# Optimization experiments

Measured on AMD Instinct MI355X. Metric: run time of the kernel, lower is better.

The kernel has to match this reference:

```python
import jax, jax.numpy as jnp
import numpy as np

# dims: batch B, seq T, model C, expert hidden H, num experts E, top-k K
B, T, C, H, E, K = 4, 1024, 1024, 1024, 8, 2


def _swiglu(x):
    a, b = jnp.split(x, 2, axis=-1)
    return jax.nn.silu(a) * b


def setup_inputs() -> dict:
    key = jax.random.key(0)
    ks = jax.random.split(key, 6)
    s = 0.02
    x = jax.random.normal(ks[0], (B, T, C), jnp.float32)
    # weights stored [in, out] (transpose of torch Linear layout; same math y = x @ W)
    w_shared_in = jax.random.normal(ks[1], (C, 2 * H), jnp.float32) * s
    w_shared_out = jax.random.normal(ks[2], (H, C), jnp.float32) * s
    w1_shared = jax.random.normal(ks[3], (C, 2 * H), jnp.float32) * s
    w2 = jax.random.normal(ks[4], (E, H, C), jnp.float32) * s  # stacked routed_w2
    w_gate = jax.random.normal(ks[5], (C, E), jnp.float32) * s
    gate_bias = jnp.zeros((E,), jnp.float32)  # buffer, updated only in training
    return {
        "x": x,
        "w_shared_in": w_shared_in,
        "w_shared_out": w_shared_out,
        "w1_shared": w1_shared,
        "w2": w2,
        "w_gate": w_gate,
        "gate_bias": gate_bias,
    }


def reference(x, w_shared_in, w_shared_out, w1_shared, w2, w_gate, gate_bias):
    Bx, Tx, Cx = x.shape
    S = Bx * Tx
    fx = x.reshape(S, Cx)  # [S, C]

    # shared expert: SwiGLU MLP
    shared_out = _swiglu(fx @ w_shared_in) @ w_shared_out  # [S, C]

    # router: softmax(top-k) over biased logits
    logits = fx @ w_gate + gate_bias  # [S, E]
    probs = jax.nn.softmax(logits, axis=-1)
    top_val, top_idx = jax.lax.top_k(probs, K)  # [S, K]

    # dense dispatch-weight matrix [S, E] (zero where expert not selected)
    wdense = jnp.zeros((S, E), probs.dtype).at[
        jnp.arange(S)[:, None], top_idx
    ].add(top_val)

    # routed experts share w1_shared, so the SwiGLU hidden is identical for all
    # experts; compute it once for every token, then apply per-expert w2.
    hid = _swiglu(fx @ w1_shared)  # [S, H]
    routed_out = jnp.zeros_like(shared_out)
    for e in range(E):  # small fixed expert count
        routed_out = routed_out + wdense[:, e:e + 1] * (hid @ w2[e])

    return (shared_out + routed_out).reshape(Bx, Tx, Cx)
```

## Files before the change

kernel.cpp:

```cpp
#include <hip/hip_runtime.h>
#include <stdint.h>

typedef __attribute__((ext_vector_type(4))) float f32x4;
typedef __attribute__((ext_vector_type(8))) short s16x8;

static constexpr int S_TOK = 4096;
static constexpr int CDIM  = 1024;
static constexpr int HDIM  = 1024;
static constexpr int H2    = 2048;
static constexpr int NEXP  = 8;

#define MAXRT2 40

__device__ __forceinline__ unsigned short f2bf(float f) {
  union { float f; uint32_t u; } c; c.f = f;
  uint32_t u = c.u;
  u += 0x7fffu + ((u >> 16) & 1u);
  return (unsigned short)(u >> 16);
}

__device__ __forceinline__ float bf2f(unsigned short u) {
  return __uint_as_float(((uint32_t)u) << 16);
}

__device__ __forceinline__ void gload16(const void* g, void* l) {
  __builtin_amdgcn_global_load_lds(
      (const __attribute__((address_space(1))) void*)g,
      (__attribute__((address_space(3))) void*)l, 16, 0, 0);
}

__global__ __launch_bounds__(256) void prep_kernel(
    const float* __restrict__ wsi, const float* __restrict__ w1s,
    const float* __restrict__ wso, const float* __restrict__ w2,
    unsigned short* __restrict__ w12i, unsigned short* __restrict__ wso_t,
    unsigned short* __restrict__ w2t) {
  __shared__ float t[32][33];
  const int b = blockIdx.x;
  const int tid = threadIdx.x;

  if (b < 4096) {
    const float* src = (b >= 2048) ? w1s : wsi;
    const int halfoff = (b >= 2048) ? 2048 : 0;
    const int rem = b & 2047;
    const int r0 = (rem >> 6) * 32;
    const int c0 = (rem & 63) * 32;
#pragma unroll
    for (int i = 0; i < 4; ++i) {
      int idx = tid + i * 256;
      int r = idx >> 5, c = idx & 31;
      t[r][c] = src[(size_t)(r0 + r) * H2 + c0 + c];
    }
    __syncthreads();
#pragma unroll
    for (int i = 0; i < 4; ++i) {
      int idx = tid + i * 256;
      int r = idx >> 5, c = idx & 31;
      const int ccol = c0 + r;
      const int part = ccol >> 10, h = ccol & 1023;
      const int drow = halfoff + (h & 15) + ((h >> 4) << 5) + (part << 4);
      w12i[(size_t)drow * CDIM + r0 + c] = f2bf(t[c][r]);
    }
    return;
  }
  const float* src;
  unsigned short* dst;
  int bx, by;
  if (b < 5120) {
    const int b3 = b - 4096;
    src = wso; dst = wso_t; by = b3 >> 5; bx = b3 & 31;
  } else {
    const int b4 = b - 5120;
    const int z = b4 >> 10;
    const int rem = b4 & 1023;
    src = w2 + (size_t)z * HDIM * CDIM;
    dst = w2t + (size_t)z * HDIM * CDIM;
    by = rem >> 5; bx = rem & 31;
  }
  const int r0 = by * 32, c0 = bx * 32;
#pragma unroll
  for (int i = 0; i < 4; ++i) {
    int idx = tid + i * 256;
    int r = idx >> 5, c = idx & 31;
    t[r][c] = src[(size_t)(r0 + r) * CDIM + c0 + c];
  }
  __syncthreads();
#pragma unroll
  for (int i = 0; i < 4; ++i) {
    int idx = tid + i * 256;
    int r = idx >> 5, c = idx & 31;
    dst[(size_t)(c0 + r) * HDIM + r0 + c] = f2bf(t[c][r]);
  }
}

__global__ void router_kernel(const float* __restrict__ x, const float* __restrict__ wg,
                              const float* __restrict__ gb,
                              int2* __restrict__ ti_e, float2* __restrict__ ti_w,
                              unsigned short* __restrict__ xb) {
  const int l = threadIdx.x & 63;
  const int wid = threadIdx.x >> 6;
  const int s = blockIdx.x * 4 + wid;
  const float* xr = x + (size_t)s * CDIM;
  unsigned short* xbr = xb + (size_t)s * CDIM;
  float acc[NEXP];
#pragma unroll
  for (int e = 0; e < NEXP; ++e) acc[e] = 0.f;
#pragma unroll
  for (int c4 = 0; c4 < CDIM / 4; c4 += 64) {
    const int i4 = c4 + l;
    const float4 xv = reinterpret_cast<const float4*>(xr)[i4];
    ushort4 o;
    o.x = f2bf(xv.x); o.y = f2bf(xv.y); o.z = f2bf(xv.z); o.w = f2bf(xv.w);
    reinterpret_cast<ushort4*>(xbr)[i4] = o;
    const float* wr_ = wg + (size_t)i4 * 4 * NEXP;
#pragma unroll
    for (int e = 0; e < NEXP; ++e)
      acc[e] += xv.x * wr_[e] + xv.y * wr_[e + NEXP] +
                xv.z * wr_[e + 2 * NEXP] + xv.w * wr_[e + 3 * NEXP];
  }
#pragma unroll
  for (int e = 0; e < NEXP; ++e) {
#pragma unroll
    for (int off = 32; off > 0; off >>= 1) acc[e] += __shfl_xor(acc[e], off);
    acc[e] += gb[e];
  }
  float m = acc[0];
#pragma unroll
  for (int e = 1; e < NEXP; ++e) m = fmaxf(m, acc[e]);
  float ex[NEXP], sum = 0.f;
#pragma unroll
  for (int e = 0; e < NEXP; ++e) { ex[e] = __expf(acc[e] - m); sum += ex[e]; }
  int i0 = 0;
#pragma unroll
  for (int e = 1; e < NEXP; ++e) if (acc[e] > acc[i0]) i0 = e;
  int i1 = (i0 == 0) ? 1 : 0;
#pragma unroll
  for (int e = 0; e < NEXP; ++e) {
    if (e == i0) continue;
    if (acc[e] > acc[i1]) i1 = e;
  }
  if (l == 0) {
    const float inv = 1.f / sum;
    ti_e[s] = make_int2(i0, i1);
    ti_w[s] = make_float2(ex[i0] * inv, ex[i1] * inv);
  }
}

__global__ __launch_bounds__(1024) void build_kernel(
    const int2* __restrict__ ti_e,
    int* __restrict__ cnt, int* __restrict__ offs,
    int* __restrict__ gidx, int2* __restrict__ ti_slot) {
  __shared__ int gcnt[64][NEXP];
  __shared__ int gbase[64][NEXP];
  __shared__ int eoff[NEXP];
  const int tid = threadIdx.x;
  const int wid = tid >> 6, lane = tid & 63;

  for (int p = 0; p < 4; ++p) {
    const int g = p * 16 + wid;
    const int2 e = ti_e[g * 64 + lane];
#pragma unroll
    for (int ex = 0; ex < NEXP; ++ex) {
      uint64_t b0 = __ballot(e.x == ex);
      uint64_t b1 = __ballot(e.y == ex);
      if (lane == 0) gcnt[g][ex] = __popcll(b0) + __popcll(b1);
    }
  }
  __syncthreads();
  if (tid < NEXP) {
    const int ex = tid;
    int a = 0;
    for (int g = 0; g < 64; ++g) { gbase[g][ex] = a; a += gcnt[g][ex]; }
    eoff[ex] = a;
  }
  __syncthreads();
  if (tid == 0) {
    int a = 0;
#pragma unroll
    for (int ex = 0; ex < NEXP; ++ex) {
      const int c = eoff[ex];
      offs[ex] = a; cnt[ex] = c; eoff[ex] = a; a += c;
    }
    offs[NEXP] = a;
  }
  __syncthreads();
  for (int p = 0; p < 4; ++p) {
    const int g = p * 16 + wid;
    const int s = g * 64 + lane;
    const int2 e = ti_e[s];
    const uint64_t below = (lane == 0) ? 0ull : (~0ull >> (64 - lane));
    const uint64_t beloweq = below | (1ull << lane);
    int slot0 = 0, slot1 = 0;
#pragma unroll
    for (int ex = 0; ex < NEXP; ++ex) {
      uint64_t b0 = __ballot(e.x == ex);
      uint64_t b1 = __ballot(e.y == ex);
      const int base = gbase[g][ex];
      if (e.x == ex) slot0 = base + __popcll(b0 & below) + __popcll(b1 & below);
      if (e.y == ex) slot1 = base + __popcll(b0 & beloweq) + __popcll(b1 & below);
    }
    ti_slot[s] = make_int2(slot0, slot1);
    gidx[eoff[e.x] + slot0] = s;
    gidx[eoff[e.y] + slot1] = s;
  }
}

__global__ __launch_bounds__(256, 4) void gemm1_kernel(
    const unsigned short* __restrict__ xb, const unsigned short* __restrict__ w12i,
    unsigned short* __restrict__ Hs, unsigned short* __restrict__ Hr) {
  __shared__ unsigned short As[128 * 32];
  __shared__ unsigned short Bs[128 * 32];
  const int tid = threadIdx.x;
  const int l = tid & 63, wid = tid >> 6;
  const int wr = wid >> 1, wc = wid & 1;
  const int lr = l & 15, lk = (l >> 4) << 3;
  const int hw = blockIdx.y * gridDim.x + blockIdx.x;
  const int logical = (hw & 7) * 128 + (hw >> 3);
  const int m0 = (logical >> 5) * 128;
  const int n0 = (logical & 31) * 128;
  f32x4 acc[4][4] = {};
  const unsigned short* ga0 = xb + (size_t)(m0 + (tid >> 2)) * CDIM + ((tid & 3) << 3);
  const unsigned short* ga1 = ga0 + (size_t)64 * CDIM;
  const unsigned short* gb0 = w12i + (size_t)(n0 + (tid >> 2)) * CDIM + ((tid & 3) << 3);
  const unsigned short* gb1 = gb0 + (size_t)64 * CDIM;

  for (int k0 = 0; k0 < 1024; k0 += 32) {
    gload16(ga0 + k0, As + tid * 8);
    gload16(ga1 + k0, As + 2048 + tid * 8);
    gload16(gb0 + k0, Bs + tid * 8);
    gload16(gb1 + k0, Bs + 2048 + tid * 8);
    __syncthreads();
    s16x8 a[4], b[4];
#pragma unroll
    for (int fm = 0; fm < 4; ++fm)
      a[fm] = *reinterpret_cast<const s16x8*>(As + (wr * 64 + fm * 16 + lr) * 32 + lk);
#pragma unroll
    for (int fn = 0; fn < 4; ++fn)
      b[fn] = *reinterpret_cast<const s16x8*>(Bs + (wc * 64 + fn * 16 + lr) * 32 + lk);
#pragma unroll
    for (int fm = 0; fm < 4; ++fm)
#pragma unroll
      for (int fn = 0; fn < 4; ++fn)
        acc[fm][fn] = __builtin_amdgcn_mfma_f32_16x16x32_bf16(a[fm], b[fn], acc[fm][fn], 0, 0, 0);
    __syncthreads();
  }

  unsigned short* Hbuf = (n0 < 2048) ? Hs : Hr;
  const int rb = m0 + wr * 64 + ((l >> 4) << 2);
  const int hb0 = ((n0 & 2047) >> 1) + wc * 32;
#pragma unroll
  for (int fm = 0; fm < 4; ++fm)
#pragma unroll
    for (int j = 0; j < 2; ++j)
#pragma unroll
      for (int r = 0; r < 4; ++r) {
        float a = acc[fm][2 * j][r];
        float b = acc[fm][2 * j + 1][r];
        float hv = (a / (1.f + __expf(-a))) * b;
        Hbuf[(size_t)(rb + fm * 16 + r) * HDIM + hb0 + j * 16 + lr] = f2bf(hv);
      }
}

__global__ __launch_bounds__(512) void gemm2_kernel(
    const unsigned short* __restrict__ Hs, const unsigned short* __restrict__ Hr,
    const unsigned short* __restrict__ wso_t, const unsigned short* __restrict__ w2t,
    const int* __restrict__ cnt, const int* __restrict__ offs, const int* __restrict__ gidx,
    unsigned short* __restrict__ Dout, unsigned short* __restrict__ Eout) {
  __shared__ unsigned short SA[4][2][4096];
  __shared__ unsigned short SB[4][2][4096];
  const int tid = threadIdx.x;
  const int l = tid & 63, wid = tid >> 6;
  const int wm = wid >> 2, wn = wid & 3;
  const int lr = l & 15;
  const int hi8 = (l >> 4) << 3;
  const int wnh = wn >> 1;
  const int wno = (wn & 1) << 6;
  const int hw = blockIdx.y * gridDim.x + blockIdx.x;
  const int logical = (hw & 7) * 28 + (hw >> 3);
  const int gx = logical >> 2;
  const int n0 = (logical & 3) * 256;
  f32x4 acc[8][4] = {};

  const int srow = tid >> 2;
  const int cs = (((tid & 3) ^ ((tid >> 3) & 3)) << 3);

  const unsigned short *pa0, *pa1, *pb0, *pb1;
  int e = 0, cnte = 0, mt = 0, base = 0;
  const bool dense = (gx < 16);
  if (dense) {
    const int m0 = gx * 256;
    pa0 = Hs + (size_t)(m0 + srow) * HDIM + cs;
    pa1 = pa0 + (size_t)128 * HDIM;
    pb0 = wso_t + (size_t)(n0 + srow) * HDIM + cs;
    pb1 = pb0 + (size_t)128 * HDIM;
  } else {
    int t = gx - 16;
    bool found = false;
#pragma unroll
    for (int ee = 0; ee < NEXP; ++ee) {
      int c = cnt[ee];
      int nt = (c + 255) >> 8;
      if (!found) {
        if (t < nt) { e = ee; cnte = c; found = true; }
        else t -= nt;
      }
    }
    if (!found) return;
    mt = t;
    base = offs[e];
    const int r0 = mt * 256 + srow;
    const int tok0 = gidx[base + min(r0, cnte - 1)];
    const int tok1 = gidx[base + min(r0 + 128, cnte - 1)];
    pa0 = Hr + (size_t)tok0 * HDIM + cs;
    pa1 = Hr + (size_t)tok1 * HDIM + cs;
    pb0 = w2t + (size_t)e * CDIM * HDIM + (size_t)(n0 + srow) * HDIM + cs;
    pb1 = pb0 + (size_t)128 * HDIM;
  }

  const int t8 = tid * 8;
#pragma unroll
  for (int s = 0; s < 3; ++s) {
    const int kk = s * 32;
    gload16(pa0 + kk, &SA[s][0][t8]);
    gload16(pa1 + kk, &SA[s][1][t8]);
    gload16(pb0 + kk, &SB[s][0][t8]);
    gload16(pb1 + kk, &SB[s][1][t8]);
  }

  for (int s = 0; s < 32; ++s) {
    if (s < 30)       asm volatile("s_waitcnt vmcnt(8)" ::: "memory");
    else if (s == 30) asm volatile("s_waitcnt vmcnt(4)" ::: "memory");
    else              asm volatile("s_waitcnt vmcnt(0)" ::: "memory");
    __builtin_amdgcn_s_barrier();
    asm volatile("" ::: "memory");
    const int c = s & 3;
    const unsigned short* A_ = &SA[c][wm][0];
    const unsigned short* B_ = &SB[c][wnh][0];
    s16x8 a[8], b[4];
#pragma unroll
    for (int f = 0; f < 8; ++f) {
      const int r = f * 16 + lr;
      a[f] = *reinterpret_cast<const s16x8*>(&A_[r * 32 + (hi8 ^ (((r >> 1) & 3) << 3))]);
    }
#pragma unroll
    for (int j = 0; j < 4; ++j) {
      const int r = wno + j * 16 + lr;
      b[j] = *reinterpret_cast<const s16x8*>(&B_[r * 32 + (hi8 ^ (((r >> 1) & 3) << 3))]);
    }
    const int c3 = (s + 3) & 3;
    const int kk = (s + 3) * 32;
    const bool st = (s <= 28);
    if (st) gload16(pa0 + kk, &SA[c3][0][t8]);
    __builtin_amdgcn_s_setprio(1);
#pragma unroll
    for (int f = 0; f < 4; ++f) {
      acc[f][0] = __builtin_amdgcn_mfma_f32_16x16x32_bf16(a[f], b[0], acc[f][0], 0, 0, 0);
      acc[f][1] = __builtin_amdgcn_mfma_f32_16x16x32_bf16(a[f], b[1], acc[f][1], 0, 0, 0);
    }
    __builtin_amdgcn_s_setprio(0);
    if (st) gload16(pa1 + kk, &SA[c3][1][t8]);
    __builtin_amdgcn_s_setprio(1);
#pragma unroll
    for (int f = 0; f < 4; ++f) {
      acc[f][2] = __builtin_amdgcn_mfma_f32_16x16x32_bf16(a[f], b[2], acc[f][2], 0, 0, 0);
      acc[f][3] = __builtin_amdgcn_mfma_f32_16x16x32_bf16(a[f], b[3], acc[f][3], 0, 0, 0);
    }
    __builtin_amdgcn_s_setprio(0);
    if (st) gload16(pb0 + kk, &SB[c3][0][t8]);
    __builtin_amdgcn_s_setprio(1);
#pragma unroll
    for (int f = 0; f < 4; ++f) {
      acc[4 + f][0] = __builtin_amdgcn_mfma_f32_16x16x32_bf16(a[4 + f], b[0], acc[4 + f][0], 0, 0, 0);
      acc[4 + f][1] = __builtin_amdgcn_mfma_f32_16x16x32_bf16(a[4 + f], b[1], acc[4 + f][1], 0, 0, 0);
    }
    __builtin_amdgcn_s_setprio(0);
    if (st) gload16(pb1 + kk, &SB[c3][1][t8]);
    __builtin_amdgcn_s_setprio(1);
#pragma unroll
    for (int f = 0; f < 4; ++f) {
      acc[4 + f][2] = __builtin_amdgcn_mfma_f32_16x16x32_bf16(a[4 + f], b[2], acc[4 + f][2], 0, 0, 0);
      acc[4 + f][3] = __builtin_amdgcn_mfma_f32_16x16x32_bf16(a[4 + f], b[3], acc[4 + f][3], 0, 0, 0);
    }
    __builtin_amdgcn_s_setprio(0);
  }

  const int rloc0 = wm * 128 + ((l >> 4) << 2);
  const int cb = n0 + wn * 64 + lr;
  if (dense) {
    const int rb = gx * 256 + rloc0;
#pragma unroll
    for (int fm = 0; fm < 8; ++fm)
#pragma unroll
      for (int fn = 0; fn < 4; ++fn)
#pragma unroll
        for (int r = 0; r < 4; ++r)
          Dout[(size_t)(rb + fm * 16 + r) * CDIM + cb + fn * 16] = f2bf(acc[fm][fn][r]);
  } else {
#pragma unroll
    for (int fm = 0; fm < 8; ++fm)
#pragma unroll
      for (int fn = 0; fn < 4; ++fn)
#pragma unroll
        for (int r = 0; r < 4; ++r) {
          const int rloc = mt * 256 + rloc0 + fm * 16 + r;
          if (rloc < cnte)
            Eout[(size_t)(base + rloc) * CDIM + cb + fn * 16] = f2bf(acc[fm][fn][r]);
        }
  }
}

__global__ void scatter_kernel(float* __restrict__ out, const unsigned short* __restrict__ Dout,
                               const unsigned short* __restrict__ Eout,
                               const int2* __restrict__ ti_e, const int2* __restrict__ ti_slot,
                               const float2* __restrict__ ti_w, const int* __restrict__ offs) {
  const int total = S_TOK * (CDIM / 8);
  int i = blockIdx.x * blockDim.x + threadIdx.x;
  const int st = gridDim.x * blockDim.x;
  for (; i < total; i += st) {
    const int s = i >> 7;
    const int j = (i & 127) << 3;
    const int2 e = ti_e[s];
    const int2 sl = ti_slot[s];
    const float2 wv = ti_w[s];
    const int p0 = offs[e.x] + sl.x;
    const int p1 = offs[e.y] + sl.y;
    const ushort4* d0 = reinterpret_cast<const ushort4*>(Dout + (size_t)s * CDIM + j);
    const ushort4* e0 = reinterpret_cast<const ushort4*>(Eout + (size_t)p0 * CDIM + j);
    const ushort4* e1 = reinterpret_cast<const ushort4*>(Eout + (size_t)p1 * CDIM + j);
    float* op = out + (size_t)s * CDIM + j;
#pragma unroll
    for (int q = 0; q < 2; ++q) {
      ushort4 dd = d0[q], a = e0[q], b = e1[q];
      float4 o;
      o.x = bf2f(dd.x) + wv.x * bf2f(a.x) + wv.y * bf2f(b.x);
      o.y = bf2f(dd.y) + wv.x * bf2f(a.y) + wv.y * bf2f(b.y);
      o.z = bf2f(dd.z) + wv.x * bf2f(a.z) + wv.y * bf2f(b.z);
      o.w = bf2f(dd.w) + wv.x * bf2f(a.w) + wv.y * bf2f(b.w);
      reinterpret_cast<float4*>(op)[q] = o;
    }
  }
}

extern "C" void kernel_launch(void* const* d_in, const int* in_sizes, int n_in,
                              void* d_out, int out_size, void* d_ws, size_t ws_size,
                              hipStream_t stream) {
  (void)in_sizes; (void)n_in; (void)out_size; (void)ws_size;
  const float* x   = (const float*)d_in[0];
  const float* wsi = (const float*)d_in[1];
  const float* wso = (const float*)d_in[2];
  const float* w1s = (const float*)d_in[3];
  const float* w2  = (const float*)d_in[4];
  const float* wg  = (const float*)d_in[5];
  const float* gb  = (const float*)d_in[6];
  float* out = (float*)d_out;

  char* w = (char*)d_ws;
  auto alloc = [&](size_t bytes) {
    char* p = w; w += (bytes + 255) & ~(size_t)255; return p;
  };
  unsigned short* xb    = (unsigned short*)alloc((size_t)S_TOK * CDIM * 2);
  unsigned short* w12i  = (unsigned short*)alloc((size_t)2 * H2 * CDIM * 2);
  unsigned short* wso_t = (unsigned short*)alloc((size_t)CDIM * HDIM * 2);
  unsigned short* w2t   = (unsigned short*)alloc((size_t)NEXP * CDIM * HDIM * 2);
  unsigned short* Hs    = (unsigned short*)alloc((size_t)S_TOK * HDIM * 2);
  unsigned short* Hr    = (unsigned short*)alloc((size_t)S_TOK * HDIM * 2);
  unsigned short* Dout  = (unsigned short*)alloc((size_t)S_TOK * CDIM * 2);
  unsigned short* Eout  = (unsigned short*)alloc((size_t)2 * S_TOK * CDIM * 2);
  int2*   ti_e   = (int2*)alloc((size_t)S_TOK * 8);
  int2*   ti_slot= (int2*)alloc((size_t)S_TOK * 8);
  float2* ti_w   = (float2*)alloc((size_t)S_TOK * 8);
  int*    cnt    = (int*)alloc(64);
  int*    offs   = (int*)alloc(64);
  int*    gidx   = (int*)alloc((size_t)2 * S_TOK * 4);

  router_kernel<<<S_TOK / 4, 256, 0, stream>>>(x, wg, gb, ti_e, ti_w, xb);
  build_kernel<<<1, 1024, 0, stream>>>(ti_e, cnt, offs, gidx, ti_slot);

  prep_kernel<<<13312, 256, 0, stream>>>(wsi, w1s, wso, w2, w12i, wso_t, w2t);

  gemm1_kernel<<<dim3(32, 32), 256, 0, stream>>>(xb, w12i, Hs, Hr);

  gemm2_kernel<<<dim3(16 + MAXRT2, CDIM / 256), 512, 0, stream>>>(
      Hs, Hr, wso_t, w2t, cnt, offs, gidx, Dout, Eout);

  scatter_kernel<<<2048, 256, 0, stream>>>(out, Dout, Eout, ti_e, ti_slot, ti_w, offs);
}
```

Baseline: 128.3 us.

## Move gemm1 onto the pipelined 256x256 gemm2 core and simplify router loads

Factors the 4-stage, swizzled-LDS, prefetch-interleaved MFMA main loop out of gemm2 into a shared device function. gemm1 now uses it with 256x256 tiles, 512 threads and a 16x16 grid, replacing its 128x128 single-buffered loop that waited on barriers every k-step. The aim is more overlap of global loads with MFMA work and more reuse per tile, at the cost of far fewer blocks (256) and possibly lower occupancy. The router loop also switches from float4 loads to scalar per-element loads, which may reduce load efficiency.

```diff
diff --git a/kernel.cpp b/kernel.cpp
--- a/kernel.cpp
+++ b/kernel.cpp
@@ -104,18 +104,12 @@
   float acc[NEXP];
 #pragma unroll
   for (int e = 0; e < NEXP; ++e) acc[e] = 0.f;
-#pragma unroll
-  for (int c4 = 0; c4 < CDIM / 4; c4 += 64) {
-    const int i4 = c4 + l;
-    const float4 xv = reinterpret_cast<const float4*>(xr)[i4];
-    ushort4 o;
-    o.x = f2bf(xv.x); o.y = f2bf(xv.y); o.z = f2bf(xv.z); o.w = f2bf(xv.w);
-    reinterpret_cast<ushort4*>(xbr)[i4] = o;
-    const float* wr_ = wg + (size_t)i4 * 4 * NEXP;
-#pragma unroll
-    for (int e = 0; e < NEXP; ++e)
-      acc[e] += xv.x * wr_[e] + xv.y * wr_[e + NEXP] +
-                xv.z * wr_[e + 2 * NEXP] + xv.w * wr_[e + 3 * NEXP];
+  for (int c = l; c < CDIM; c += 64) {
+    float xv = xr[c];
+    xbr[c] = f2bf(xv);
+    const float* wr_ = wg + (size_t)c * NEXP;
+#pragma unroll
+    for (int e = 0; e < NEXP; ++e) acc[e] += xv * wr_[e];
   }
 #pragma unroll
   for (int e = 0; e < NEXP; ++e) {
@@ -204,59 +198,118 @@
   }
 }
 
-__global__ __launch_bounds__(256, 4) void gemm1_kernel(
+__device__ __forceinline__ void core_d3(
+    const unsigned short* pa0, const unsigned short* pa1,
+    const unsigned short* pb0, const unsigned short* pb1,
+    unsigned short* SA, unsigned short* SB,
+    int tid, int wm, int wnh, int wno, int lr, int hi8,
+    f32x4 (&acc)[8][4]) {
+  const int t8 = tid * 8;
+#pragma unroll
+  for (int s = 0; s < 3; ++s) {
+    const int kk = s * 32;
+    gload16(pa0 + kk, SA + s * 8192 + t8);
+    gload16(pa1 + kk, SA + s * 8192 + 4096 + t8);
+    gload16(pb0 + kk, SB + s * 8192 + t8);
+    gload16(pb1 + kk, SB + s * 8192 + 4096 + t8);
+  }
+  for (int s = 0; s < 32; ++s) {
+    if (s < 30)       asm volatile("s_waitcnt vmcnt(8)" ::: "memory");
+    else if (s == 30) asm volatile("s_waitcnt vmcnt(4)" ::: "memory");
+    else              asm volatile("s_waitcnt vmcnt(0)" ::: "memory");
+    __builtin_amdgcn_s_barrier();
+    asm volatile("" ::: "memory");
+    const int c = s & 3;
+    const unsigned short* A_ = SA + c * 8192 + wm * 4096;
+    const unsigned short* B_ = SB + c * 8192 + wnh * 4096;
+    s16x8 a[8], b[4];
+#pragma unroll
+    for (int f = 0; f < 8; ++f) {
+      const int r = f * 16 + lr;
+      a[f] = *reinterpret_cast<const s16x8*>(&A_[r * 32 + (hi8 ^ (((r >> 1) & 3) << 3))]);
+    }
+#pragma unroll
+    for (int j = 0; j < 4; ++j) {
+      const int r = wno + j * 16 + lr;
+      b[j] = *reinterpret_cast<const s16x8*>(&B_[r * 32 + (hi8 ^ (((r >> 1) & 3) << 3))]);
+    }
+    const int c3 = (s + 3) & 3;
+    const int kk = (s + 3) * 32;
+    const bool st = (s <= 28);
+    if (st) gload16(pa0 + kk, SA + c3 * 8192 + t8);
+    __builtin_amdgcn_s_setprio(1);
+#pragma unroll
+    for (int f = 0; f < 4; ++f) {
+      acc[f][0] = __builtin_amdgcn_mfma_f32_16x16x32_bf16(a[f], b[0], acc[f][0], 0, 0, 0);
+      acc[f][1] = __builtin_amdgcn_mfma_f32_16x16x32_bf16(a[f], b[1], acc[f][1], 0, 0, 0);
+    }
+    __builtin_amdgcn_s_setprio(0);
+    if (st) gload16(pa1 + kk, SA + c3 * 8192 + 4096 + t8);
+    __builtin_amdgcn_s_setprio(1);
+#pragma unroll
+    for (int f = 0; f < 4; ++f) {
+      acc[f][2] = __builtin_amdgcn_mfma_f32_16x16x32_bf16(a[f], b[2], acc[f][2], 0, 0, 0);
+      acc[f][3] = __builtin_amdgcn_mfma_f32_16x16x32_bf16(a[f], b[3], acc[f][3], 0, 0, 0);
+    }
+    __builtin_amdgcn_s_setprio(0);
+    if (st) gload16(pb0 + kk, SB + c3 * 8192 + t8);
+    __builtin_amdgcn_s_setprio(1);
+#pragma unroll
+    for (int f = 0; f < 4; ++f) {
+      acc[4 + f][0] = __builtin_amdgcn_mfma_f32_16x16x32_bf16(a[4 + f], b[0], acc[4 + f][0], 0, 0, 0);
+      acc[4 + f][1] = __builtin_amdgcn_mfma_f32_16x16x32_bf16(a[4 + f], b[1], acc[4 + f][1], 0, 0, 0);
+    }
+    __builtin_amdgcn_s_setprio(0);
+    if (st) gload16(pb1 + kk, SB + c3 * 8192 + 4096 + t8);
+    __builtin_amdgcn_s_setprio(1);
+#pragma unroll
+    for (int f = 0; f < 4; ++f) {
+      acc[4 + f][2] = __builtin_amdgcn_mfma_f32_16x16x32_bf16(a[4 + f], b[2], acc[4 + f][2], 0, 0, 0);
+      acc[4 + f][3] = __builtin_amdgcn_mfma_f32_16x16x32_bf16(a[4 + f], b[3], acc[4 + f][3], 0, 0, 0);
+    }
+    __builtin_amdgcn_s_setprio(0);
+  }
+}
+
+__global__ __launch_bounds__(512) void gemm1_kernel(
     const unsigned short* __restrict__ xb, const unsigned short* __restrict__ w12i,
     unsigned short* __restrict__ Hs, unsigned short* __restrict__ Hr) {
-  __shared__ unsigned short As[128 * 32];
-  __shared__ unsigned short Bs[128 * 32];
+  __shared__ unsigned short SA[4 * 2 * 4096];
+  __shared__ unsigned short SB[4 * 2 * 4096];
   const int tid = threadIdx.x;
   const int l = tid & 63, wid = tid >> 6;
-  const int wr = wid >> 1, wc = wid & 1;
-  const int lr = l & 15, lk = (l >> 4) << 3;
+  const int wm = wid >> 2, wn = wid & 3;
+  const int lr = l & 15;
+  const int hi8 = (l >> 4) << 3;
+  const int wnh = wn >> 1;
+  const int wno = (wn & 1) << 6;
   const int hw = blockIdx.y * gridDim.x + blockIdx.x;
-  const int logical = (hw & 7) * 128 + (hw >> 3);
-  const int m0 = (logical >> 5) * 128;
-  const int n0 = (logical & 31) * 128;
-  f32x4 acc[4][4] = {};
-  const unsigned short* ga0 = xb + (size_t)(m0 + (tid >> 2)) * CDIM + ((tid & 3) << 3);
-  const unsigned short* ga1 = ga0 + (size_t)64 * CDIM;
-  const unsigned short* gb0 = w12i + (size_t)(n0 + (tid >> 2)) * CDIM + ((tid & 3) << 3);
-  const unsigned short* gb1 = gb0 + (size_t)64 * CDIM;
-
-  for (int k0 = 0; k0 < 1024; k0 += 32) {
-    gload16(ga0 + k0, As + tid * 8);
-    gload16(ga1 + k0, As + 2048 + tid * 8);
-    gload16(gb0 + k0, Bs + tid * 8);
-    gload16(gb1 + k0, Bs + 2048 + tid * 8);
-    __syncthreads();
-    s16x8 a[4], b[4];
-#pragma unroll
-    for (int fm = 0; fm < 4; ++fm)
-      a[fm] = *reinterpret_cast<const s16x8*>(As + (wr * 64 + fm * 16 + lr) * 32 + lk);
-#pragma unroll
-    for (int fn = 0; fn < 4; ++fn)
-      b[fn] = *reinterpret_cast<const s16x8*>(Bs + (wc * 64 + fn * 16 + lr) * 32 + lk);
-#pragma unroll
-    for (int fm = 0; fm < 4; ++fm)
-#pragma unroll
-      for (int fn = 0; fn < 4; ++fn)
-        acc[fm][fn] = __builtin_amdgcn_mfma_f32_16x16x32_bf16(a[fm], b[fn], acc[fm][fn], 0, 0, 0);
-    __syncthreads();
-  }
+  const int logical = (hw & 7) * 32 + (hw >> 3);
+  const int m0 = (logical >> 4) * 256;
+  const int n0 = (logical & 15) * 256;
+  const int srow = tid >> 2;
+  const int cs = (((tid & 3) ^ ((tid >> 3) & 3)) << 3);
+  f32x4 acc[8][4] = {};
+  const unsigned short* pa0 = xb + (size_t)(m0 + srow) * CDIM + cs;
+  const unsigned short* pa1 = pa0 + (size_t)128 * CDIM;
+  const unsigned short* pb0 = w12i + (size_t)(n0 + srow) * CDIM + cs;
+  const unsigned short* pb1 = pb0 + (size_t)128 * CDIM;
+
+  core_d3(pa0, pa1, pb0, pb1, SA, SB, tid, wm, wnh, wno, lr, hi8, acc);
 
   unsigned short* Hbuf = (n0 < 2048) ? Hs : Hr;
-  const int rb = m0 + wr * 64 + ((l >> 4) << 2);
-  const int hb0 = ((n0 & 2047) >> 1) + wc * 32;
-#pragma unroll
-  for (int fm = 0; fm < 4; ++fm)
+  const int rb = m0 + wm * 128 + ((l >> 4) << 2);
+  const int hbase = ((n0 & 2047) >> 1) + wn * 32;
+#pragma unroll
+  for (int fm = 0; fm < 8; ++fm)
 #pragma unroll
     for (int j = 0; j < 2; ++j)
 #pragma unroll
       for (int r = 0; r < 4; ++r) {
-        float a = acc[fm][2 * j][r];
-        float b = acc[fm][2 * j + 1][r];
-        float hv = (a / (1.f + __expf(-a))) * b;
-        Hbuf[(size_t)(rb + fm * 16 + r) * HDIM + hb0 + j * 16 + lr] = f2bf(hv);
+        float av = acc[fm][2 * j][r];
+        float bv = acc[fm][2 * j + 1][r];
+        float hv = (av / (1.f + __expf(-av))) * bv;
+        Hbuf[(size_t)(rb + fm * 16 + r) * HDIM + hbase + j * 16 + lr] = f2bf(hv);
       }
 }
 
@@ -265,8 +318,8 @@
     const unsigned short* __restrict__ wso_t, const unsigned short* __restrict__ w2t,
     const int* __restrict__ cnt, const int* __restrict__ offs, const int* __restrict__ gidx,
     unsigned short* __restrict__ Dout, unsigned short* __restrict__ Eout) {
-  __shared__ unsigned short SA[4][2][4096];
-  __shared__ unsigned short SB[4][2][4096];
+  __shared__ unsigned short SA[4 * 2 * 4096];
+  __shared__ unsigned short SB[4 * 2 * 4096];
   const int tid = threadIdx.x;
   const int l = tid & 63, wid = tid >> 6;
   const int wm = wid >> 2, wn = wid & 3;
@@ -316,72 +369,7 @@
     pb1 = pb0 + (size_t)128 * HDIM;
   }
 
-  const int t8 = tid * 8;
-#pragma unroll
-  for (int s = 0; s < 3; ++s) {
-    const int kk = s * 32;
-    gload16(pa0 + kk, &SA[s][0][t8]);
-    gload16(pa1 + kk, &SA[s][1][t8]);
-    gload16(pb0 + kk, &SB[s][0][t8]);
-    gload16(pb1 + kk, &SB[s][1][t8]);
-  }
-
-  for (int s = 0; s < 32; ++s) {
-    if (s < 30)       asm volatile("s_waitcnt vmcnt(8)" ::: "memory");
-    else if (s == 30) asm volatile("s_waitcnt vmcnt(4)" ::: "memory");
-    else              asm volatile("s_waitcnt vmcnt(0)" ::: "memory");
-    __builtin_amdgcn_s_barrier();
-    asm volatile("" ::: "memory");
-    const int c = s & 3;
-    const unsigned short* A_ = &SA[c][wm][0];
-    const unsigned short* B_ = &SB[c][wnh][0];
-    s16x8 a[8], b[4];
-#pragma unroll
-    for (int f = 0; f < 8; ++f) {
-      const int r = f * 16 + lr;
-      a[f] = *reinterpret_cast<const s16x8*>(&A_[r * 32 + (hi8 ^ (((r >> 1) & 3) << 3))]);
-    }
-#pragma unroll
-    for (int j = 0; j < 4; ++j) {
-      const int r = wno + j * 16 + lr;
-      b[j] = *reinterpret_cast<const s16x8*>(&B_[r * 32 + (hi8 ^ (((r >> 1) & 3) << 3))]);
-    }
-    const int c3 = (s + 3) & 3;
-    const int kk = (s + 3) * 32;
-    const bool st = (s <= 28);
-    if (st) gload16(pa0 + kk, &SA[c3][0][t8]);
-    __builtin_amdgcn_s_setprio(1);
-#pragma unroll
-    for (int f = 0; f < 4; ++f) {
-      acc[f][0] = __builtin_amdgcn_mfma_f32_16x16x32_bf16(a[f], b[0], acc[f][0], 0, 0, 0);
-      acc[f][1] = __builtin_amdgcn_mfma_f32_16x16x32_bf16(a[f], b[1], acc[f][1], 0, 0, 0);
-    }
-    __builtin_amdgcn_s_setprio(0);
-    if (st) gload16(pa1 + kk, &SA[c3][1][t8]);
-    __builtin_amdgcn_s_setprio(1);
-#pragma unroll
-    for (int f = 0; f < 4; ++f) {
-      acc[f][2] = __builtin_amdgcn_mfma_f32_16x16x32_bf16(a[f], b[2], acc[f][2], 0, 0, 0);
-      acc[f][3] = __builtin_amdgcn_mfma_f32_16x16x32_bf16(a[f], b[3], acc[f][3], 0, 0, 0);
-    }
-    __builtin_amdgcn_s_setprio(0);
-    if (st) gload16(pb0 + kk, &SB[c3][0][t8]);
-    __builtin_amdgcn_s_setprio(1);
-#pragma unroll
-    for (int f = 0; f < 4; ++f) {
-      acc[4 + f][0] = __builtin_amdgcn_mfma_f32_16x16x32_bf16(a[4 + f], b[0], acc[4 + f][0], 0, 0, 0);
-      acc[4 + f][1] = __builtin_amdgcn_mfma_f32_16x16x32_bf16(a[4 + f], b[1], acc[4 + f][1], 0, 0, 0);
-    }
-    __builtin_amdgcn_s_setprio(0);
-    if (st) gload16(pb1 + kk, &SB[c3][1][t8]);
-    __builtin_amdgcn_s_setprio(1);
-#pragma unroll
-    for (int f = 0; f < 4; ++f) {
-      acc[4 + f][2] = __builtin_amdgcn_mfma_f32_16x16x32_bf16(a[4 + f], b[2], acc[4 + f][2], 0, 0, 0);
-      acc[4 + f][3] = __builtin_amdgcn_mfma_f32_16x16x32_bf16(a[4 + f], b[3], acc[4 + f][3], 0, 0, 0);
-    }
-    __builtin_amdgcn_s_setprio(0);
-  }
+  core_d3(pa0, pa1, pb0, pb1, SA, SB, tid, wm, wnh, wno, lr, hi8, acc);
 
   const int rloc0 = wm * 128 + ((l >> 4) << 2);
   const int cb = n0 + wn * 64 + lr;
@@ -477,7 +465,7 @@
 
   prep_kernel<<<13312, 256, 0, stream>>>(wsi, w1s, wso, w2, w12i, wso_t, w2t);
 
-  gemm1_kernel<<<dim3(32, 32), 256, 0, stream>>>(xb, w12i, Hs, Hr);
+  gemm1_kernel<<<dim3(16, 16), 512, 0, stream>>>(xb, w12i, Hs, Hr);
 
   gemm2_kernel<<<dim3(16 + MAXRT2, CDIM / 256), 512, 0, stream>>>(
       Hs, Hr, wso_t, w2t, cnt, offs, gidx, Dout, Eout);
```

New measurement: 114.3 us (median of 3 runs). 1.12x faster.
